# Optimization experiments

Hardware: AMD Instinct MI355X
Metric: run time of the kernel (lower is better)

The kernel has to match this reference:

```python
import jax, jax.numpy as jnp
import numpy as np

N_NODES = 50000
N_EDGES = 800000
IN_DIM = 8
HID = 32
HEADS = 4
D1 = HID * HEADS  # 128


def setup_inputs() -> dict:
    key = jax.random.key(0)
    ks = jax.random.split(key, 10)
    x = jax.random.normal(ks[0], (N_NODES, IN_DIM), dtype=jnp.float32)
    edge_index = jax.random.randint(ks[1], (2, N_EDGES), 0, N_NODES, dtype=jnp.int64)
    s = lambda fan_in: 1.0 / np.sqrt(fan_in)
    W1 = jax.random.uniform(ks[2], (IN_DIM, D1), jnp.float32, -s(IN_DIM), s(IN_DIM))
    a1 = jax.random.uniform(ks[3], (2 * D1, 1), jnp.float32, -s(2 * D1), s(2 * D1))
    W2 = jax.random.uniform(ks[4], (D1, HID), jnp.float32, -s(D1), s(D1))
    a2 = jax.random.uniform(ks[5], (2 * HID, 1), jnp.float32, -s(2 * HID), s(2 * HID))
    hw1 = jax.random.uniform(ks[6], (HID, 32), jnp.float32, -s(HID), s(HID))
    hb1 = jax.random.uniform(ks[7], (32,), jnp.float32, -s(HID), s(HID))
    hw2 = jax.random.uniform(ks[8], (32, 1), jnp.float32, -s(32), s(32))
    hb2 = jax.random.uniform(ks[9], (1,), jnp.float32, -s(32), s(32))
    return {"x": x, "edge_index": edge_index, "W1": W1, "a1": a1,
            "W2": W2, "a2": a2, "hw1": hw1, "hb1": hb1, "hw2": hw2, "hb2": hb2}


def gat_layer(h, src, dst, W, a, n_nodes):
    # Wh: [N, D]; attention vector split so logits are computed per-node then gathered
    Wh = h @ W
    D = Wh.shape[-1]
    a_src, a_dst = a[:D, 0], a[D:, 0]
    # alpha = LeakyReLU([Wh[src] || Wh[dst]] @ a)  (same math, no [E, 2D] concat)
    alpha = jax.nn.leaky_relu((Wh @ a_src)[src] + (Wh @ a_dst)[dst], negative_slope=0.2)
    alpha_exp = jnp.exp(alpha - alpha.max())  # global-max shift, as in the original
    alpha_sum = jax.ops.segment_sum(alpha_exp, dst, num_segments=n_nodes)
    alpha_norm = alpha_exp / (alpha_sum[dst] + 1e-9)
    out = jax.ops.segment_sum(alpha_norm[:, None] * Wh[src], dst, num_segments=n_nodes)
    return jax.nn.elu(out), alpha_norm


def reference(x, edge_index, W1, a1, W2, a2, hw1, hb1, hw2, hb2):
    src, dst = edge_index[0], edge_index[1]
    n = x.shape[0]
    h, _ = gat_layer(x, src, dst, W1, a1, n)
    h, _ = gat_layer(h, src, dst, W2, a2, n)
    # head: Linear -> GELU -> (Dropout: identity in eval) -> Linear
    z = jax.nn.gelu(h @ hw1 + hb1, approximate=False)
    node_scores = (z @ hw2 + hb2).squeeze(-1)
    return node_scores
```

## Files before the change

kernel.cpp:

```cpp
#include <hip/hip_runtime.h>
#include <math.h>

#define N_NODES 50000
#define IN_DIM 8
#define HID 32
#define D1 128

#define CAP 64

#define FG 8
#define FB 128
#define GRANGE (N_NODES / FG)
#define FILL_BLOCKS (FG * FB)
#define SD1_BLOCKS ((N_NODES + 255) / 256)

__global__ void k_fill_sd1(const int* __restrict__ src, const int* __restrict__ dst,
                           int* __restrict__ cnt, int* __restrict__ esrc,
                           const float* __restrict__ x, const float* __restrict__ W1,
                           const float* __restrict__ a1,
                           float* __restrict__ s1, float* __restrict__ d1,
                           int n_edges) {
    __shared__ float bs[IN_DIM], bd[IN_DIM];
    const int t = threadIdx.x;
    if (blockIdx.x < FILL_BLOCKS) {
        const int g = blockIdx.x & (FG - 1);
        const int blk = blockIdx.x >> 3;
        const int lo = g * GRANGE, hi = lo + GRANGE;
        const int base = blk * blockDim.x + t;
        const int step = FB * blockDim.x;
        for (int i = base; i * 4 < n_edges; i += step) {
            const int4 d4 = *(const int4*)&dst[i * 4];
            const bool mx = d4.x >= lo && d4.x < hi;
            const bool my = d4.y >= lo && d4.y < hi;
            const bool mz = d4.z >= lo && d4.z < hi;
            const bool mw = d4.w >= lo && d4.w < hi;
            if (mx | my | mz | mw) {
                const int4 s4 = *(const int4*)&src[i * 4];
                if (mx) { const int p = atomicAdd(&cnt[d4.x], 1); if (p < CAP) esrc[d4.x * CAP + p] = s4.x; }
                if (my) { const int p = atomicAdd(&cnt[d4.y], 1); if (p < CAP) esrc[d4.y * CAP + p] = s4.y; }
                if (mz) { const int p = atomicAdd(&cnt[d4.z], 1); if (p < CAP) esrc[d4.z * CAP + p] = s4.z; }
                if (mw) { const int p = atomicAdd(&cnt[d4.w], 1); if (p < CAP) esrc[d4.w * CAP + p] = s4.w; }
            }
        }
    } else {
        if (t < 16) {
            const int k = t & 7;
            const float* av = a1 + ((t < 8) ? 0 : D1);
            float acc = 0.f;
            for (int j = 0; j < D1; ++j) acc += W1[k * D1 + j] * av[j];
            if (t < 8) bs[k] = acc; else bd[k] = acc;
        }
        __syncthreads();
        const int node = (blockIdx.x - FILL_BLOCKS) * blockDim.x + t;
        if (node >= N_NODES) return;
        const float4 x0 = *(const float4*)&x[node * 8];
        const float4 x1 = *(const float4*)&x[node * 8 + 4];
        s1[node] = x0.x*bs[0] + x0.y*bs[1] + x0.z*bs[2] + x0.w*bs[3]
                 + x1.x*bs[4] + x1.y*bs[5] + x1.z*bs[6] + x1.w*bs[7];
        d1[node] = x0.x*bd[0] + x0.y*bd[1] + x0.z*bd[2] + x0.w*bd[3]
                 + x1.x*bd[4] + x1.y*bd[5] + x1.z*bd[6] + x1.w*bd[7];
    }
}

__global__ void k_aggr_x(const int* __restrict__ esrc, const int* __restrict__ cnt,
                         const float* __restrict__ s, const float* __restrict__ d,
                         const float* __restrict__ x, float* __restrict__ xa) {
    const int w = (blockIdx.x * blockDim.x + threadIdx.x) >> 6;
    const int lane = threadIdx.x & 63;
    const int half = lane >> 5, sub = lane & 31;
    const int node = w * 2 + half;
    if (node >= N_NODES) return;
    const int start = node * CAP;
    const int deg = cnt[node];
    const float dn = d[node];
    const int slot = sub >> 1;
    const int cp = sub & 1;
    float4 acc = {0.f, 0.f, 0.f, 0.f};
    float wsum = 0.f;
    for (int idx = slot; idx < deg; idx += 16) {
        const int se = esrc[start + idx];
        float a = s[se] + dn;
        a = a > 0.f ? a : 0.2f * a;
        const float ww = expf(a);
        const float4 v = *(const float4*)&x[se * IN_DIM + cp * 4];
        acc.x += ww * v.x;  acc.y += ww * v.y;
        acc.z += ww * v.z;  acc.w += ww * v.w;
        wsum += ww;
    }
#pragma unroll
    for (int off = 2; off < 32; off <<= 1) {
        acc.x += __shfl_xor(acc.x, off);
        acc.y += __shfl_xor(acc.y, off);
        acc.z += __shfl_xor(acc.z, off);
        acc.w += __shfl_xor(acc.w, off);
        wsum  += __shfl_xor(wsum, off);
    }
    const float inv = 1.f / (wsum + 1e-9f);
    acc.x *= inv;  acc.y *= inv;  acc.z *= inv;  acc.w *= inv;
    if (sub < 2) *(float4*)&xa[node * IN_DIM + sub * 4] = acc;
}

__global__ void k_node_mid(const float* __restrict__ xa,
                           const float* __restrict__ W1,
                           const float* __restrict__ W2,
                           const float* __restrict__ a2,
                           float* __restrict__ Wh2,
                           float* __restrict__ s2, float* __restrict__ d2) {
    const int tid = blockIdx.x * blockDim.x + threadIdx.x;
    const int node = tid >> 2;
    const int q = tid & 3;
    if (node >= N_NODES) return;
    const float4 x0 = *(const float4*)&xa[node * 8];
    const float4 x1 = *(const float4*)&xa[node * 8 + 4];
    float acc[8];
#pragma unroll
    for (int j = 0; j < 8; ++j) acc[j] = 0.f;
    const float* W2q = W2 + q * 8;
#pragma unroll 4
    for (int k = 0; k < D1; ++k) {
        float h = x0.x * W1[0 * D1 + k] + x0.y * W1[1 * D1 + k]
                + x0.z * W1[2 * D1 + k] + x0.w * W1[3 * D1 + k]
                + x1.x * W1[4 * D1 + k] + x1.y * W1[5 * D1 + k]
                + x1.z * W1[6 * D1 + k] + x1.w * W1[7 * D1 + k];
        h = h > 0.f ? h : (expf(h) - 1.f);
        const float4 w0 = *(const float4*)&W2q[k * HID];
        const float4 w1 = *(const float4*)&W2q[k * HID + 4];
        acc[0] += h * w0.x;  acc[1] += h * w0.y;
        acc[2] += h * w0.z;  acc[3] += h * w0.w;
        acc[4] += h * w1.x;  acc[5] += h * w1.y;
        acc[6] += h * w1.z;  acc[7] += h * w1.w;
    }
    float ss = 0.f, dd = 0.f;
#pragma unroll
    for (int j = 0; j < 8; ++j) {
        ss += acc[j] * a2[q * 8 + j];
        dd += acc[j] * a2[HID + q * 8 + j];
    }
    ss += __shfl_xor(ss, 1);  ss += __shfl_xor(ss, 2);
    dd += __shfl_xor(dd, 1);  dd += __shfl_xor(dd, 2);
    if (q == 0) { s2[node] = ss; d2[node] = dd; }
    float4* o = (float4*)&Wh2[node * HID + q * 8];
    o[0] = make_float4(acc[0], acc[1], acc[2], acc[3]);
    o[1] = make_float4(acc[4], acc[5], acc[6], acc[7]);
}

__global__ void k_aggr32_head(const int* __restrict__ esrc, const int* __restrict__ cnt,
                              const float* __restrict__ s, const float* __restrict__ d,
                              const float* __restrict__ Wh,
                              const float* __restrict__ hw1, const float* __restrict__ hb1,
                              const float* __restrict__ hw2, const float* __restrict__ hb2,
                              float* __restrict__ scores) {
    const int w = (blockIdx.x * blockDim.x + threadIdx.x) >> 6;
    const int lane = threadIdx.x & 63;
    const int half = lane >> 5, sub = lane & 31, base = lane & 32;
    const int node = w * 2 + half;
    if (node >= N_NODES) return;
    const int start = node * CAP;
    const int deg = cnt[node];
    const float dn = d[node];
    const int slot = sub >> 3;
    const int cp = sub & 7;
    float4 acc = {0.f, 0.f, 0.f, 0.f};
    float wsum = 0.f;
    for (int idx = slot; idx < deg; idx += 4) {
        const int se = esrc[start + idx];
        float a = s[se] + dn;
        a = a > 0.f ? a : 0.2f * a;
        const float ww = expf(a);
        const float4 v = *(const float4*)&Wh[se * HID + cp * 4];
        acc.x += ww * v.x;  acc.y += ww * v.y;
        acc.z += ww * v.z;  acc.w += ww * v.w;
        wsum += ww;
    }
#pragma unroll
    for (int off = 8; off < 32; off <<= 1) {
        acc.x += __shfl_xor(acc.x, off);
        acc.y += __shfl_xor(acc.y, off);
        acc.z += __shfl_xor(acc.z, off);
        acc.w += __shfl_xor(acc.w, off);
        wsum  += __shfl_xor(wsum, off);
    }
    const float inv = 1.f / (wsum + 1e-9f);
    acc.x *= inv;  acc.y *= inv;  acc.z *= inv;  acc.w *= inv;
    const int srcl = base + (sub >> 2);
    const float g0 = __shfl(acc.x, srcl);
    const float g1 = __shfl(acc.y, srcl);
    const float g2 = __shfl(acc.z, srcl);
    const float g3 = __shfl(acc.w, srcl);
    const int r = sub & 3;
    float v = (r == 0) ? g0 : (r == 1) ? g1 : (r == 2) ? g2 : g3;
    const float h = v > 0.f ? v : (expf(v) - 1.f);
    float z = hb1[sub];
#pragma unroll
    for (int k = 0; k < HID; ++k) {
        const float hk = __shfl(h, base + k);
        z += hk * hw1[k * HID + sub];
    }
    z = 0.5f * z * (1.f + erff(z * 0.7071067811865475f));
    float sc = z * hw2[sub];
#pragma unroll
    for (int off = 16; off > 0; off >>= 1) sc += __shfl_xor(sc, off);
    if (sub == 0) scores[node] = sc + hb2[0];
}

extern "C" void kernel_launch(void* const* d_in, const int* in_sizes, int n_in,
                              void* d_out, int out_size, void* d_ws, size_t ws_size,
                              hipStream_t stream) {
    const float* x   = (const float*)d_in[0];
    const int*   ei  = (const int*)d_in[1];
    const float* W1  = (const float*)d_in[2];
    const float* a1  = (const float*)d_in[3];
    const float* W2  = (const float*)d_in[4];
    const float* a2  = (const float*)d_in[5];
    const float* hw1 = (const float*)d_in[6];
    const float* hb1 = (const float*)d_in[7];
    const float* hw2 = (const float*)d_in[8];
    const float* hb2 = (const float*)d_in[9];
    float* out = (float*)d_out;

    const int n_edges = in_sizes[1] / 2;
    const int* src = ei;
    const int* dst = ei + n_edges;

    float* p = (float*)d_ws;
    float* xa   = p; p += (size_t)N_NODES * IN_DIM;
    float* Wh2  = p; p += (size_t)N_NODES * HID;
    float* s1   = p; p += N_NODES;
    float* d1   = p; p += N_NODES;
    float* s2   = p; p += N_NODES;
    float* d2   = p; p += N_NODES;
    int* cnt    = (int*)p; p += N_NODES;
    int* esrc   = (int*)p; p += (size_t)N_NODES * CAP;

    hipMemsetAsync(cnt, 0, N_NODES * sizeof(int), stream);

    const int AGGR_BLOCKS = (N_NODES * 32 + 255) / 256;

    k_fill_sd1<<<FILL_BLOCKS + SD1_BLOCKS, 256, 0, stream>>>(
        src, dst, cnt, esrc, x, W1, a1, s1, d1, n_edges);

    k_aggr_x<<<AGGR_BLOCKS, 256, 0, stream>>>(esrc, cnt, s1, d1, x, xa);

    k_node_mid<<<(N_NODES * 4 + 255) / 256, 256, 0, stream>>>(xa, W1, W2, a2, Wh2, s2, d2);
    k_aggr32_head<<<AGGR_BLOCKS, 256, 0, stream>>>(esrc, cnt, s2, d2, Wh2,
                                                   hw1, hb1, hw2, hb2, out);
}
```

Before: 188.4 us.

## Fuse layer-1 aggregation with mid-node transform into one kernel via shared memory

Merges the layer-1 edge aggregation kernel and the per-node W1/ELU/W2 transform kernel into one kernel. Aggregated features for 8 nodes per block go through shared memory instead of a global xa buffer, and the 128-wide hidden vector is staged in LDS. Each thread then computes one output column with a 32-lane reduction for s2/d2. This removes a kernel launch and the xa round trip, at the cost of block-wide syncs and the removal of the node bounds check. The bounds check is not needed because N_NODES divides evenly by 8.

```diff
diff --git a/kernel.cpp b/kernel.cpp
--- a/kernel.cpp
+++ b/kernel.cpp
@@ -62,14 +62,21 @@
     }
 }
 
-__global__ void k_aggr_x(const int* __restrict__ esrc, const int* __restrict__ cnt,
-                         const float* __restrict__ s, const float* __restrict__ d,
-                         const float* __restrict__ x, float* __restrict__ xa) {
-    const int w = (blockIdx.x * blockDim.x + threadIdx.x) >> 6;
-    const int lane = threadIdx.x & 63;
+__global__ void k_aggr_mid(const int* __restrict__ esrc, const int* __restrict__ cnt,
+                           const float* __restrict__ s, const float* __restrict__ d,
+                           const float* __restrict__ x,
+                           const float* __restrict__ W1, const float* __restrict__ W2,
+                           const float* __restrict__ a2,
+                           float* __restrict__ Wh2,
+                           float* __restrict__ s2, float* __restrict__ d2) {
+    __shared__ float xa_s[8][IN_DIM];
+    __shared__ float h_s[8][D1];
+    const int t = threadIdx.x;
+    const int wv = t >> 6;
+    const int lane = t & 63;
     const int half = lane >> 5, sub = lane & 31;
-    const int node = w * 2 + half;
-    if (node >= N_NODES) return;
+    const int nodeBase = blockIdx.x * 8;
+    const int node = nodeBase + wv * 2 + half;
     const int start = node * CAP;
     const int deg = cnt[node];
     const float dn = d[node];
@@ -96,52 +103,42 @@
         wsum  += __shfl_xor(wsum, off);
     }
     const float inv = 1.f / (wsum + 1e-9f);
-    acc.x *= inv;  acc.y *= inv;  acc.z *= inv;  acc.w *= inv;
-    if (sub < 2) *(float4*)&xa[node * IN_DIM + sub * 4] = acc;
-}
-
-__global__ void k_node_mid(const float* __restrict__ xa,
-                           const float* __restrict__ W1,
-                           const float* __restrict__ W2,
-                           const float* __restrict__ a2,
-                           float* __restrict__ Wh2,
-                           float* __restrict__ s2, float* __restrict__ d2) {
-    const int tid = blockIdx.x * blockDim.x + threadIdx.x;
-    const int node = tid >> 2;
-    const int q = tid & 3;
-    if (node >= N_NODES) return;
-    const float4 x0 = *(const float4*)&xa[node * 8];
-    const float4 x1 = *(const float4*)&xa[node * 8 + 4];
-    float acc[8];
-#pragma unroll
-    for (int j = 0; j < 8; ++j) acc[j] = 0.f;
-    const float* W2q = W2 + q * 8;
-#pragma unroll 4
-    for (int k = 0; k < D1; ++k) {
-        float h = x0.x * W1[0 * D1 + k] + x0.y * W1[1 * D1 + k]
-                + x0.z * W1[2 * D1 + k] + x0.w * W1[3 * D1 + k]
-                + x1.x * W1[4 * D1 + k] + x1.y * W1[5 * D1 + k]
-                + x1.z * W1[6 * D1 + k] + x1.w * W1[7 * D1 + k];
-        h = h > 0.f ? h : (expf(h) - 1.f);
-        const float4 w0 = *(const float4*)&W2q[k * HID];
-        const float4 w1 = *(const float4*)&W2q[k * HID + 4];
-        acc[0] += h * w0.x;  acc[1] += h * w0.y;
-        acc[2] += h * w0.z;  acc[3] += h * w0.w;
-        acc[4] += h * w1.x;  acc[5] += h * w1.y;
-        acc[6] += h * w1.z;  acc[7] += h * w1.w;
-    }
-    float ss = 0.f, dd = 0.f;
-#pragma unroll
-    for (int j = 0; j < 8; ++j) {
-        ss += acc[j] * a2[q * 8 + j];
-        dd += acc[j] * a2[HID + q * 8 + j];
-    }
-    ss += __shfl_xor(ss, 1);  ss += __shfl_xor(ss, 2);
-    dd += __shfl_xor(dd, 1);  dd += __shfl_xor(dd, 2);
-    if (q == 0) { s2[node] = ss; d2[node] = dd; }
-    float4* o = (float4*)&Wh2[node * HID + q * 8];
-    o[0] = make_float4(acc[0], acc[1], acc[2], acc[3]);
-    o[1] = make_float4(acc[4], acc[5], acc[6], acc[7]);
+    if (sub < 2) {
+        float4 o;
+        o.x = acc.x * inv; o.y = acc.y * inv;
+        o.z = acc.z * inv; o.w = acc.w * inv;
+        *(float4*)&xa_s[wv * 2 + half][sub * 4] = o;
+    }
+    __syncthreads();
+    const int nloc = t >> 5;
+    const int col = t & 31;
+    const float xa0 = xa_s[nloc][0], xa1 = xa_s[nloc][1];
+    const float xa2 = xa_s[nloc][2], xa3 = xa_s[nloc][3];
+    const float xa4 = xa_s[nloc][4], xa5 = xa_s[nloc][5];
+    const float xa6 = xa_s[nloc][6], xa7 = xa_s[nloc][7];
+#pragma unroll
+    for (int j = 0; j < 4; ++j) {
+        const int k = col + 32 * j;
+        float h = xa0 * W1[0 * D1 + k] + xa1 * W1[1 * D1 + k]
+                + xa2 * W1[2 * D1 + k] + xa3 * W1[3 * D1 + k]
+                + xa4 * W1[4 * D1 + k] + xa5 * W1[5 * D1 + k]
+                + xa6 * W1[6 * D1 + k] + xa7 * W1[7 * D1 + k];
+        h_s[nloc][k] = h > 0.f ? h : (expf(h) - 1.f);
+    }
+    __syncthreads();
+    float o = 0.f;
+#pragma unroll 8
+    for (int k = 0; k < D1; ++k) o += h_s[nloc][k] * W2[k * HID + col];
+    float ss = o * a2[col];
+    float dd = o * a2[HID + col];
+#pragma unroll
+    for (int off = 1; off < 32; off <<= 1) {
+        ss += __shfl_xor(ss, off);
+        dd += __shfl_xor(dd, off);
+    }
+    const int node2 = nodeBase + nloc;
+    Wh2[node2 * HID + col] = o;
+    if (col == 0) { s2[node2] = ss; d2[node2] = dd; }
 }
 
 __global__ void k_aggr32_head(const int* __restrict__ esrc, const int* __restrict__ cnt,
@@ -223,7 +220,6 @@
     const int* dst = ei + n_edges;
 
     float* p = (float*)d_ws;
-    float* xa   = p; p += (size_t)N_NODES * IN_DIM;
     float* Wh2  = p; p += (size_t)N_NODES * HID;
     float* s1   = p; p += N_NODES;
     float* d1   = p; p += N_NODES;
@@ -239,9 +235,9 @@
     k_fill_sd1<<<FILL_BLOCKS + SD1_BLOCKS, 256, 0, stream>>>(
         src, dst, cnt, esrc, x, W1, a1, s1, d1, n_edges);
 
-    k_aggr_x<<<AGGR_BLOCKS, 256, 0, stream>>>(esrc, cnt, s1, d1, x, xa);
-
-    k_node_mid<<<(N_NODES * 4 + 255) / 256, 256, 0, stream>>>(xa, W1, W2, a2, Wh2, s2, d2);
+    k_aggr_mid<<<(N_NODES + 7) / 8, 256, 0, stream>>>(esrc, cnt, s1, d1, x,
+                                                      W1, W2, a2, Wh2, s2, d2);
+
     k_aggr32_head<<<AGGR_BLOCKS, 256, 0, stream>>>(esrc, cnt, s2, d2, Wh2,
                                                    hw1, hb1, hw2, hb2, out);
 }
```

Measured after the change: 182.3 us. 3.2% less time.
